# Performance work log

Hardware: AMD Instinct MI355X
Metric: run time of the kernel (lower is better)

## Reference

```python
import jax, jax.numpy as jnp
import numpy as np

N = 50000
E = 800000
D_IN, D_HID, D_OUT = 128, 128, 64


def setup_inputs() -> dict:
    key = jax.random.key(0)
    ks = jax.random.split(key, 8)
    x = jax.random.normal(ks[0], (N, D_IN), dtype=jnp.float32)
    edge_index = jax.random.randint(ks[1], (2, E), 0, N, dtype=jnp.int64)
    # Glorot-ish init for weights
    W1 = jax.random.normal(ks[2], (D_IN, D_HID), dtype=jnp.float32) / np.sqrt(D_IN)
    b1 = jnp.zeros((D_HID,), dtype=jnp.float32)
    W2 = jax.random.normal(ks[3], (D_HID, D_OUT), dtype=jnp.float32) / np.sqrt(D_HID)
    b2 = jnp.zeros((D_OUT,), dtype=jnp.float32)
    fc_W = jax.random.normal(ks[4], (D_OUT, D_OUT), dtype=jnp.float32) / np.sqrt(D_OUT)
    fc_b = jnp.zeros((D_OUT,), dtype=jnp.float32)
    return {"x": x, "edge_index": edge_index, "W1": W1, "b1": b1,
            "W2": W2, "b2": b2, "fc_W": fc_W, "fc_b": fc_b}


def _gcn_norm(edge_index, n_nodes):
    # PyG GCNConv default: add self-loops, symmetric normalization
    src, dst = edge_index[0], edge_index[1]
    loops = jnp.arange(n_nodes, dtype=edge_index.dtype)
    src = jnp.concatenate([src, loops])
    dst = jnp.concatenate([dst, loops])
    deg = jax.ops.segment_sum(jnp.ones_like(dst, dtype=jnp.float32), dst,
                              num_segments=n_nodes)
    dinv = jnp.where(deg > 0, jax.lax.rsqrt(deg), 0.0)
    norm = dinv[src] * dinv[dst]  # [E + N]
    return src, dst, norm


def _gcn_conv(x, src, dst, norm, W, b):
    h = x @ W                          # [N, d_out] transform first (fewer FLOPs)
    msg = h[src] * norm[:, None]       # gather + scale  [E+N, d_out]
    out = jax.ops.segment_sum(msg, dst, num_segments=x.shape[0])
    return out + b


def reference(x, edge_index, W1, b1, W2, b2, fc_W, fc_b):
    src, dst, norm = _gcn_norm(edge_index, x.shape[0])
    h = jax.nn.relu(_gcn_conv(x, src, dst, norm, W1, b1))
    h = jax.nn.relu(_gcn_conv(h, src, dst, norm, W2, b2))
    return h @ fc_W + fc_b
```

## Files before the change

### kernel.cpp

```cpp
#include <hip/hip_runtime.h>
#include <hip/hip_bf16.h>


typedef __attribute__((ext_vector_type(8))) short bf16x8;
typedef __attribute__((ext_vector_type(4))) float f32x4;

#define SLAB 64
#define BCAP 6144
#define BINCH 4096
#define BINR (BINCH / 1024)

__device__ __forceinline__ unsigned short f2bf(float f) {
    unsigned u = __float_as_uint(f);
    unsigned r = (u + 0x7FFFu + ((u >> 16) & 1u)) >> 16;
    return (unsigned short)r;
}
__device__ __forceinline__ float bf16_lo(unsigned u) {
    return __uint_as_float((u & 0xFFFFu) << 16);
}
__device__ __forceinline__ float bf16_hi(unsigned u) {
    return __uint_as_float(u & 0xFFFF0000u);
}

#define UNPK16(cA, cB, ci)                                        \
    ci[0] = cA.x & 0xFFFFu;  ci[1] = cA.x >> 16;                  \
    ci[2] = cA.y & 0xFFFFu;  ci[3] = cA.y >> 16;                  \
    ci[4] = cA.z & 0xFFFFu;  ci[5] = cA.z >> 16;                  \
    ci[6] = cA.w & 0xFFFFu;  ci[7] = cA.w >> 16;                  \
    ci[8] = cB.x & 0xFFFFu;  ci[9] = cB.x >> 16;                  \
    ci[10] = cB.y & 0xFFFFu; ci[11] = cB.y >> 16;                 \
    ci[12] = cB.z & 0xFFFFu; ci[13] = cB.z >> 16;                 \
    ci[14] = cB.w & 0xFFFFu; ci[15] = cB.w >> 16;


__global__ void k_wt(const float* __restrict__ W1, const float* __restrict__ W2,
                     const float* __restrict__ fcW,
                     unsigned short* __restrict__ W1T, unsigned short* __restrict__ W2T,
                     unsigned short* __restrict__ fcWT, int* __restrict__ gcnt,
                     unsigned short* __restrict__ hs1r, unsigned short* __restrict__ hs2,
                     int n) {
    int j = blockIdx.x * blockDim.x + threadIdx.x;
    if (j < 256) gcnt[j] = 0;
    if (j < 16384) {
        int m = j >> 7, k = j & 127;
        W1T[j] = f2bf(W1[k * 128 + m]);
    } else if (j < 24576) {
        int q = j - 16384;
        int m = q >> 7, k = q & 127;
        W2T[q] = f2bf(W2[k * 64 + m]);
    } else if (j < 28672) {
        int q = j - 24576;
        int m = q >> 6, k = q & 63;
        fcWT[q] = f2bf(fcW[k * 64 + m]);
    } else if (j < 28800) {
        hs1r[(size_t)n * 128 + (j - 28672)] = 0;
    } else if (j < 28864) {
        hs2[(size_t)n * 64 + (j - 28800)] = 0;
    }
}


__device__ __forceinline__ void gemm1_body(const float* __restrict__ X,
                                           const unsigned short* __restrict__ W1T,
                                           unsigned short* __restrict__ outp,
                                           int n, int blk, int tid,
                                           unsigned short* xs) {
    constexpr int LDW = 136;
    int base = blk * 64;
    for (int idx = tid; idx < 64 * 32; idx += 256) {
        int r = idx >> 5, c = idx & 31;
        int row = base + r;
        float4 v = make_float4(0.f, 0.f, 0.f, 0.f);
        if (row < n) v = ((const float4*)X)[(size_t)row * 32 + c];
        unsigned short* dp = &xs[r * LDW + c * 4];
        dp[0] = f2bf(v.x); dp[1] = f2bf(v.y); dp[2] = f2bf(v.z); dp[3] = f2bf(v.w);
    }
    __syncthreads();

    int wave = tid >> 6, lane = tid & 63;
    int quad = lane >> 4, l16 = lane & 15;
    int rbase = wave * 16;

    bf16x8 af[4];
#pragma unroll
    for (int kb = 0; kb < 4; ++kb)
        af[kb] = *(const bf16x8*)&xs[(rbase + l16) * LDW + kb * 32 + quad * 8];

    f32x4 accs[8];
#pragma unroll
    for (int jt = 0; jt < 8; ++jt) {
        f32x4 acc = {0.f, 0.f, 0.f, 0.f};
#pragma unroll
        for (int kb = 0; kb < 4; ++kb) {
            bf16x8 bf = *(const bf16x8*)&W1T[(size_t)(jt * 16 + l16) * 128 + kb * 32 + quad * 8];
            acc = __builtin_amdgcn_mfma_f32_16x16x32_bf16(af[kb], bf, acc, 0, 0, 0);
        }
        accs[jt] = acc;
    }
    __syncthreads();

#pragma unroll
    for (int jt = 0; jt < 8; ++jt)
#pragma unroll
        for (int r = 0; r < 4; ++r)
            xs[(rbase + quad * 4 + r) * LDW + jt * 16 + l16] = f2bf(accs[jt][r]);
    __syncthreads();
    for (int idx = tid; idx < 64 * 16; idx += 256) {
        int r = idx >> 4, cc = idx & 15;
        int row = base + r;
        if (row < n) {
            uint4 v = *(const uint4*)&xs[r * LDW + cc * 8];
            *(uint4*)&outp[(size_t)row * 128 + cc * 8] = v;
        }
    }
}


__global__ __launch_bounds__(1024) void k_front(
    const int* __restrict__ src, const int* __restrict__ dst, int e,
    int* __restrict__ gcnt, unsigned* __restrict__ staging,
    const float* __restrict__ x, const unsigned short* __restrict__ W1T,
    unsigned short* __restrict__ hs1r, int n, int nbk, int ngemm) {
    __shared__ __align__(16) unsigned short xs4[4][64 * 136];
    __shared__ int bcnt[256], bpos[256], gofs[256];
    int bid = (int)blockIdx.x, tid = (int)threadIdx.x;

    if (bid < ngemm) {
        int tile = tid >> 8;
        gemm1_body(x, W1T, hs1r, n, bid * 4 + tile, tid & 255, xs4[tile]);
    } else {
        int b0 = bid - ngemm;
        if (tid < 256) { bcnt[tid] = 0; bpos[tid] = 0; }
        __syncthreads();
        int e0 = b0 * BINCH;
        int d[BINR], s[BINR];
#pragma unroll
        for (int r = 0; r < BINR; ++r) {
            int i = e0 + r * 1024 + tid;
            if (i < e) { d[r] = dst[i]; s[r] = src[i]; } else d[r] = -1;
        }
#pragma unroll
        for (int r = 0; r < BINR; ++r)
            if (d[r] >= 0) atomicAdd(&bcnt[d[r] >> 8], 1);
        __syncthreads();
        if (tid < nbk) {
            int c = bcnt[tid];
            gofs[tid] = c ? atomicAdd(&gcnt[tid], c) : 0;
        }
        __syncthreads();
#pragma unroll
        for (int r = 0; r < BINR; ++r) {
            if (d[r] >= 0) {
                int b = d[r] >> 8;
                int p = atomicAdd(&bpos[b], 1);
                int idx = gofs[b] + p;
                if (idx < BCAP)
                    staging[(size_t)b * BCAP + idx] =
                        ((unsigned)d[r] << 16) | (unsigned)s[r];
            }
        }
    }
}


__global__ __launch_bounds__(1024) void k_scatter(
    const unsigned* __restrict__ staging, const int* __restrict__ gcnt,
    int* __restrict__ cnt, unsigned short* __restrict__ col,
    float* __restrict__ dinv, unsigned* __restrict__ hs1u, int n) {
    __shared__ int lcnt[256];
    __shared__ __align__(16) unsigned short ls[256 * SLAB];
    __shared__ float sdi[256];
    int b = (int)blockIdx.x, t = (int)threadIdx.x;
    if (t < 256) lcnt[t] = 0;
    unsigned sent2 = (unsigned)n | ((unsigned)n << 16);
    for (int i = t; i < 256 * SLAB / 2; i += 1024) ((unsigned*)ls)[i] = sent2;
    __syncthreads();
    int eb = gcnt[b]; if (eb > BCAP) eb = BCAP;
    const unsigned* sp = staging + (size_t)b * BCAP;
    for (int i = t; i < eb; i += 1024) {
        unsigned pk = sp[i];
        int dl = (int)(pk >> 16) & 255;
        int pos = atomicAdd(&lcnt[dl], 1);
        if (pos < SLAB) ls[(dl << 6) + pos] = (unsigned short)(pk & 0xFFFFu);
    }
    __syncthreads();
    int base = b << 8;
    const uint4* lsv = (const uint4*)ls;
    uint4* gv = (uint4*)(col + ((size_t)base << 6));
    for (int i = t; i < 256 * SLAB / 8; i += 1024) gv[i] = lsv[i];
    if (t < 256) {
        int c = lcnt[t];
        float dv = rsqrtf((float)c + 1.0f);
        sdi[t] = dv;
        cnt[base + t] = c;
        dinv[base + t] = dv;
    }
    __syncthreads();
    int rows = n - base; if (rows > 256) rows = 256; if (rows < 0) rows = 0;
    unsigned* hp = hs1u + ((size_t)base << 6);
    for (int i = t; i < rows * 64; i += 1024) {
        int r = i >> 6;
        unsigned u = hp[i];
        float sc = sdi[r];
        unsigned lo = f2bf(sc * bf16_lo(u));
        unsigned hi = f2bf(sc * bf16_hi(u));
        hp[i] = lo | (hi << 16);
    }
}


__global__ __launch_bounds__(256) void k_aggg128(
    const int* __restrict__ cnt, const unsigned short* __restrict__ col,
    const unsigned short* __restrict__ hs, const float* __restrict__ dinv,
    const float* __restrict__ bias, const unsigned short* __restrict__ W2T,
    unsigned short* __restrict__ hs2, int n) {
    __shared__ __align__(16) unsigned short ys[16 * 136];
    __shared__ float ldi[16];
    int tid = (int)threadIdx.x;
    int w = tid >> 6, lane = tid & 63;
    int q = lane >> 4, l16 = lane & 15;
    int gbase = (int)blockIdx.x * 16;
    const uint4* hp4 = (const uint4*)hs;

    int node = gbase + w * 4 + q;
    int c = cnt[node]; if (c > SLAB) c = SLAB;

    const unsigned short* cp = &col[(size_t)node * SLAB];
    float di = dinv[node];
    int h0 = node < n ? node : n;
    uint4 su = hp4[(size_t)h0 * 16 + l16];
    float a0 = bf16_lo(su.x), a1 = bf16_hi(su.x);
    float a2 = bf16_lo(su.y), a3 = bf16_hi(su.y);
    float a4 = bf16_lo(su.z), a5 = bf16_hi(su.z);
    float a6 = bf16_lo(su.w), a7 = bf16_hi(su.w);

    uint4 cA = *(const uint4*)&cp[0];
    uint4 cB = *(const uint4*)&cp[8];
    for (int i = 0; i < c; i += 16) {
        int nx = (i + 16) & 63;
        uint4 nA = *(const uint4*)&cp[nx];
        uint4 nB = *(const uint4*)&cp[nx + 8];
        unsigned ci[16];
        UNPK16(cA, cB, ci)
        uint4 u[16];
#pragma unroll
        for (int j = 0; j < 16; ++j) u[j] = hp4[(size_t)ci[j] * 16 + l16];
#pragma unroll
        for (int j = 0; j < 16; ++j) {
            a0 += bf16_lo(u[j].x); a1 += bf16_hi(u[j].x);
            a2 += bf16_lo(u[j].y); a3 += bf16_hi(u[j].y);
            a4 += bf16_lo(u[j].z); a5 += bf16_hi(u[j].z);
            a6 += bf16_lo(u[j].w); a7 += bf16_hi(u[j].w);
        }
        cA = nA; cB = nB;
    }

    float4 bv0 = *(const float4*)&bias[l16 * 8];
    float4 bv1 = *(const float4*)&bias[l16 * 8 + 4];
    float v0 = fmaxf(di * a0 + bv0.x, 0.0f);
    float v1 = fmaxf(di * a1 + bv0.y, 0.0f);
    float v2 = fmaxf(di * a2 + bv0.z, 0.0f);
    float v3 = fmaxf(di * a3 + bv0.w, 0.0f);
    float v4 = fmaxf(di * a4 + bv1.x, 0.0f);
    float v5 = fmaxf(di * a5 + bv1.y, 0.0f);
    float v6 = fmaxf(di * a6 + bv1.z, 0.0f);
    float v7 = fmaxf(di * a7 + bv1.w, 0.0f);
    uint4 ov;
    ov.x = (unsigned)f2bf(v0) | ((unsigned)f2bf(v1) << 16);
    ov.y = (unsigned)f2bf(v2) | ((unsigned)f2bf(v3) << 16);
    ov.z = (unsigned)f2bf(v4) | ((unsigned)f2bf(v5) << 16);
    ov.w = (unsigned)f2bf(v6) | ((unsigned)f2bf(v7) << 16);
    *(uint4*)((char*)ys + (size_t)(w * 4 + q) * 272 + l16 * 16) = ov;
    if (l16 == 0) ldi[w * 4 + q] = di;
    __syncthreads();

    int quad = lane >> 4, l16b = lane & 15;
    bf16x8 a[4];
#pragma unroll
    for (int kb = 0; kb < 4; ++kb)
        a[kb] = *(const bf16x8*)&ys[l16b * 136 + kb * 32 + quad * 8];
    f32x4 acc = {0.f, 0.f, 0.f, 0.f};
#pragma unroll
    for (int kb = 0; kb < 4; ++kb) {
        bf16x8 bf = *(const bf16x8*)&W2T[(size_t)(w * 16 + l16b) * 128 + kb * 32 + quad * 8];
        acc = __builtin_amdgcn_mfma_f32_16x16x32_bf16(a[kb], bf, acc, 0, 0, 0);
    }
#pragma unroll
    for (int r = 0; r < 4; ++r) {
        int lrow = quad * 4 + r;
        int row = gbase + lrow;
        if (row < n)
            hs2[(size_t)row * 64 + w * 16 + l16b] = f2bf(acc[r] * ldi[lrow]);
    }
}


__global__ __launch_bounds__(256) void k_aggg64(
    const int* __restrict__ cnt, const unsigned short* __restrict__ col,
    const unsigned short* __restrict__ hs, const float* __restrict__ dinv,
    const float* __restrict__ bias, const unsigned short* __restrict__ fcWT,
    const float* __restrict__ fcb, float* __restrict__ out, int n) {
    __shared__ __align__(16) unsigned short yt[16 * 72];
    int tid = (int)threadIdx.x;
    int w = tid >> 6, lane = tid & 63;
    int q = lane >> 4, l16 = lane & 15;
    int gbase = (int)blockIdx.x * 16;
    const uint2* hp2 = (const uint2*)hs;

    int node = gbase + w * 4 + q;
    int c = cnt[node]; if (c > SLAB) c = SLAB;

    const unsigned short* cp = &col[(size_t)node * SLAB];
    float di = dinv[node];
    int h0 = node < n ? node : n;
    uint2 su = hp2[(size_t)h0 * 16 + l16];
    float a0 = bf16_lo(su.x), a1 = bf16_hi(su.x);
    float a2 = bf16_lo(su.y), a3 = bf16_hi(su.y);

    uint4 cA = *(const uint4*)&cp[0];
    uint4 cB = *(const uint4*)&cp[8];
    for (int i = 0; i < c; i += 16) {
        int nx = (i + 16) & 63;
        uint4 nA = *(const uint4*)&cp[nx];
        uint4 nB = *(const uint4*)&cp[nx + 8];
        unsigned ci[16];
        UNPK16(cA, cB, ci)
        uint2 u[16];
#pragma unroll
        for (int j = 0; j < 16; ++j) u[j] = hp2[(size_t)ci[j] * 16 + l16];
#pragma unroll
        for (int j = 0; j < 16; ++j) {
            a0 += bf16_lo(u[j].x); a1 += bf16_hi(u[j].x);
            a2 += bf16_lo(u[j].y); a3 += bf16_hi(u[j].y);
        }
        cA = nA; cB = nB;
    }

    float4 bv = *(const float4*)&bias[l16 * 4];
    float v0 = fmaxf(di * a0 + bv.x, 0.0f);
    float v1 = fmaxf(di * a1 + bv.y, 0.0f);
    float v2 = fmaxf(di * a2 + bv.z, 0.0f);
    float v3 = fmaxf(di * a3 + bv.w, 0.0f);
    uint2 ov;
    ov.x = (unsigned)f2bf(v0) | ((unsigned)f2bf(v1) << 16);
    ov.y = (unsigned)f2bf(v2) | ((unsigned)f2bf(v3) << 16);
    *(uint2*)((char*)yt + (size_t)(w * 4 + q) * 144 + l16 * 8) = ov;
    __syncthreads();

    int quad = lane >> 4, l16b = lane & 15;
    bf16x8 a[2];
#pragma unroll
    for (int kb = 0; kb < 2; ++kb)
        a[kb] = *(const bf16x8*)&yt[l16b * 72 + kb * 32 + quad * 8];
    f32x4 acc = {0.f, 0.f, 0.f, 0.f};
#pragma unroll
    for (int kb = 0; kb < 2; ++kb) {
        bf16x8 bf = *(const bf16x8*)&fcWT[(size_t)(w * 16 + l16b) * 64 + kb * 32 + quad * 8];
        acc = __builtin_amdgcn_mfma_f32_16x16x32_bf16(a[kb], bf, acc, 0, 0, 0);
    }
    float bv2 = fcb[w * 16 + l16b];
#pragma unroll
    for (int r = 0; r < 4; ++r) {
        int row = gbase + quad * 4 + r;
        if (row < n)
            out[(size_t)row * 64 + w * 16 + l16b] = acc[r] + bv2;
    }
}


extern "C" void kernel_launch(void* const* d_in, const int* in_sizes, int n_in,
                              void* d_out, int out_size, void* d_ws, size_t ws_size,
                              hipStream_t stream) {
    const float* x   = (const float*)d_in[0];
    const int*   ei  = (const int*)d_in[1];
    const float* W1  = (const float*)d_in[2];
    const float* b1  = (const float*)d_in[3];
    const float* W2  = (const float*)d_in[4];
    const float* b2  = (const float*)d_in[5];
    const float* fcW = (const float*)d_in[6];
    const float* fcb = (const float*)d_in[7];
    float* out = (float*)d_out;

    const int N = in_sizes[0] / 128;
    const int E = in_sizes[1] / 2;
    const int* src = ei;
    const int* dst = ei + E;

    const int NB    = (N + 255) >> 8;
    const int Npad  = NB << 8;
    const int nbin  = (E + BINCH - 1) / BINCH;
    const int gg64  = (N + 63) / 64;
    const int ngemm = (gg64 + 3) / 4;
    const int nagg  = (N + 15) / 16;

    auto align16 = [](size_t v) { return (v + 15) & ~(size_t)15; };
    char* p = (char*)d_ws;
    int* gcnt = (int*)p;                       p += align16(sizeof(int) * 256);
    unsigned* staging = (unsigned*)p;          p += align16(sizeof(unsigned) * (size_t)NB * BCAP);
    int* cnt = (int*)p;                        p += align16(sizeof(int) * Npad);
    float* dinv = (float*)p;                   p += align16(sizeof(float) * Npad);
    unsigned short* col = (unsigned short*)p;  p += align16(sizeof(unsigned short) * (size_t)Npad * SLAB);
    unsigned short* W1T = (unsigned short*)p;  p += align16(2 * 128 * 128);
    unsigned short* W2T = (unsigned short*)p;  p += align16(2 * 64 * 128);
    unsigned short* fcWT = (unsigned short*)p; p += align16(2 * 64 * 64);
    unsigned short* hs1r = (unsigned short*)p; p += align16(2 * ((size_t)N + 1) * 128);
    unsigned short* hs2 = (unsigned short*)p;  p += align16(2 * ((size_t)N + 1) * 64);

    k_wt<<<114, 256, 0, stream>>>(W1, W2, fcW, W1T, W2T, fcWT, gcnt,
                                  hs1r, hs2, N);

    k_front<<<ngemm + nbin, 1024, 0, stream>>>(src, dst, E, gcnt, staging,
                                               x, W1T, hs1r, N, NB, ngemm);
    k_scatter<<<NB, 1024, 0, stream>>>(staging, gcnt, cnt, col, dinv,
                                       (unsigned*)hs1r, N);

    k_aggg128<<<nagg, 256, 0, stream>>>(cnt, col, hs1r, dinv, b1, W2T, hs2, N);

    k_aggg64<<<nagg, 256, 0, stream>>>(cnt, col, hs2, dinv, b2, fcWT, fcb, out, N);
}
```

Measured before the change: 172.2 us.

## Regroup preprocessing: fuse edge binning with weight prep, GEMM with CSR scatter

```diff
diff --git a/kernel.cpp b/kernel.cpp
--- a/kernel.cpp
+++ b/kernel.cpp
@@ -33,29 +33,66 @@
     ci[14] = cB.w & 0xFFFFu; ci[15] = cB.w >> 16;
 
 
-__global__ void k_wt(const float* __restrict__ W1, const float* __restrict__ W2,
-                     const float* __restrict__ fcW,
-                     unsigned short* __restrict__ W1T, unsigned short* __restrict__ W2T,
-                     unsigned short* __restrict__ fcWT, int* __restrict__ gcnt,
-                     unsigned short* __restrict__ hs1r, unsigned short* __restrict__ hs2,
-                     int n) {
-    int j = blockIdx.x * blockDim.x + threadIdx.x;
-    if (j < 256) gcnt[j] = 0;
-    if (j < 16384) {
-        int m = j >> 7, k = j & 127;
-        W1T[j] = f2bf(W1[k * 128 + m]);
-    } else if (j < 24576) {
-        int q = j - 16384;
-        int m = q >> 7, k = q & 127;
-        W2T[q] = f2bf(W2[k * 64 + m]);
-    } else if (j < 28672) {
-        int q = j - 24576;
-        int m = q >> 6, k = q & 63;
-        fcWT[q] = f2bf(fcW[k * 64 + m]);
-    } else if (j < 28800) {
-        hs1r[(size_t)n * 128 + (j - 28672)] = 0;
-    } else if (j < 28864) {
-        hs2[(size_t)n * 64 + (j - 28800)] = 0;
+__global__ __launch_bounds__(1024) void k_init(
+    const int* __restrict__ src, const int* __restrict__ dst, int e,
+    int* __restrict__ gcnt, unsigned* __restrict__ staging,
+    const float* __restrict__ W1, const float* __restrict__ W2,
+    const float* __restrict__ fcW,
+    unsigned short* __restrict__ W1T, unsigned short* __restrict__ W2T,
+    unsigned short* __restrict__ fcWT,
+    unsigned short* __restrict__ hs1r, unsigned short* __restrict__ hs2,
+    int n, int nbk, int nbin) {
+    __shared__ int bcnt[256], bpos[256], gofs[256];
+    int bid = (int)blockIdx.x, tid = (int)threadIdx.x;
+
+    if (bid < nbin) {
+        if (tid < 256) { bcnt[tid] = 0; bpos[tid] = 0; }
+        __syncthreads();
+        int e0 = bid * BINCH;
+        int d[BINR], s[BINR];
+#pragma unroll
+        for (int r = 0; r < BINR; ++r) {
+            int i = e0 + r * 1024 + tid;
+            if (i < e) { d[r] = dst[i]; s[r] = src[i]; } else d[r] = -1;
+        }
+#pragma unroll
+        for (int r = 0; r < BINR; ++r)
+            if (d[r] >= 0) atomicAdd(&bcnt[d[r] >> 8], 1);
+        __syncthreads();
+        if (tid < nbk) {
+            int c = bcnt[tid];
+            gofs[tid] = c ? atomicAdd(&gcnt[tid], c) : 0;
+        }
+        __syncthreads();
+#pragma unroll
+        for (int r = 0; r < BINR; ++r) {
+            if (d[r] >= 0) {
+                int b = d[r] >> 8;
+                int p = atomicAdd(&bpos[b], 1);
+                int idx = gofs[b] + p;
+                if (idx < BCAP)
+                    staging[(size_t)b * BCAP + idx] =
+                        ((unsigned)d[r] << 16) | (unsigned)s[r];
+            }
+        }
+    } else {
+        int j = (bid - nbin) * 1024 + tid;
+        if (j < 16384) {
+            int m = j >> 7, k = j & 127;
+            W1T[j] = f2bf(W1[k * 128 + m]);
+        } else if (j < 24576) {
+            int q = j - 16384;
+            int m = q >> 7, k = q & 127;
+            W2T[q] = f2bf(W2[k * 64 + m]);
+        } else if (j < 28672) {
+            int q = j - 24576;
+            int m = q >> 6, k = q & 63;
+            fcWT[q] = f2bf(fcW[k * 64 + m]);
+        } else if (j < 28800) {
+            hs1r[(size_t)n * 128 + (j - 28672)] = 0;
+        } else if (j < 28864) {
+            hs2[(size_t)n * 64 + (j - 28800)] = 0;
+        }
     }
 }
 
@@ -116,95 +153,45 @@
 }
 
 
-__global__ __launch_bounds__(1024) void k_front(
-    const int* __restrict__ src, const int* __restrict__ dst, int e,
-    int* __restrict__ gcnt, unsigned* __restrict__ staging,
+__global__ __launch_bounds__(1024) void k_gemsc(
     const float* __restrict__ x, const unsigned short* __restrict__ W1T,
-    unsigned short* __restrict__ hs1r, int n, int nbk, int ngemm) {
-    __shared__ __align__(16) unsigned short xs4[4][64 * 136];
-    __shared__ int bcnt[256], bpos[256], gofs[256];
+    unsigned short* __restrict__ hs1r,
+    const unsigned* __restrict__ staging, const int* __restrict__ gcnt,
+    int* __restrict__ cnt, unsigned short* __restrict__ col,
+    float* __restrict__ dinv, int n, int ngemm) {
+    __shared__ __align__(16) unsigned char smem[69632];
     int bid = (int)blockIdx.x, tid = (int)threadIdx.x;
 
     if (bid < ngemm) {
         int tile = tid >> 8;
-        gemm1_body(x, W1T, hs1r, n, bid * 4 + tile, tid & 255, xs4[tile]);
+        unsigned short* xs = (unsigned short*)(smem + tile * 17408);
+        gemm1_body(x, W1T, hs1r, n, bid * 4 + tile, tid & 255, xs);
     } else {
-        int b0 = bid - ngemm;
-        if (tid < 256) { bcnt[tid] = 0; bpos[tid] = 0; }
+        int* lcnt = (int*)smem;
+        unsigned short* ls = (unsigned short*)(smem + 1024);
+        int b = bid - ngemm, t = tid;
+        if (t < 256) lcnt[t] = 0;
+        unsigned sent2 = (unsigned)n | ((unsigned)n << 16);
+        for (int i = t; i < 256 * SLAB / 2; i += 1024) ((unsigned*)ls)[i] = sent2;
         __syncthreads();
-        int e0 = b0 * BINCH;
-        int d[BINR], s[BINR];
-#pragma unroll
-        for (int r = 0; r < BINR; ++r) {
-            int i = e0 + r * 1024 + tid;
-            if (i < e) { d[r] = dst[i]; s[r] = src[i]; } else d[r] = -1;
-        }
-#pragma unroll
-        for (int r = 0; r < BINR; ++r)
-            if (d[r] >= 0) atomicAdd(&bcnt[d[r] >> 8], 1);
+        int eb = gcnt[b]; if (eb > BCAP) eb = BCAP;
+        const unsigned* sp = staging + (size_t)b * BCAP;
+        for (int i = t; i < eb; i += 1024) {
+            unsigned pk = sp[i];
+            int dl = (int)(pk >> 16) & 255;
+            int pos = atomicAdd(&lcnt[dl], 1);
+            if (pos < SLAB) ls[(dl << 6) + pos] = (unsigned short)(pk & 0xFFFFu);
+        }
         __syncthreads();
-        if (tid < nbk) {
-            int c = bcnt[tid];
-            gofs[tid] = c ? atomicAdd(&gcnt[tid], c) : 0;
-        }
-        __syncthreads();
-#pragma unroll
-        for (int r = 0; r < BINR; ++r) {
-            if (d[r] >= 0) {
-                int b = d[r] >> 8;
-                int p = atomicAdd(&bpos[b], 1);
-                int idx = gofs[b] + p;
-                if (idx < BCAP)
-                    staging[(size_t)b * BCAP + idx] =
-                        ((unsigned)d[r] << 16) | (unsigned)s[r];
-            }
-        }
-    }
-}
-
-
-__global__ __launch_bounds__(1024) void k_scatter(
-    const unsigned* __restrict__ staging, const int* __restrict__ gcnt,
-    int* __restrict__ cnt, unsigned short* __restrict__ col,
-    float* __restrict__ dinv, unsigned* __restrict__ hs1u, int n) {
-    __shared__ int lcnt[256];
-    __shared__ __align__(16) unsigned short ls[256 * SLAB];
-    __shared__ float sdi[256];
-    int b = (int)blockIdx.x, t = (int)threadIdx.x;
-    if (t < 256) lcnt[t] = 0;
-    unsigned sent2 = (unsigned)n | ((unsigned)n << 16);
-    for (int i = t; i < 256 * SLAB / 2; i += 1024) ((unsigned*)ls)[i] = sent2;
-    __syncthreads();
-    int eb = gcnt[b]; if (eb > BCAP) eb = BCAP;
-    const unsigned* sp = staging + (size_t)b * BCAP;
-    for (int i = t; i < eb; i += 1024) {
-        unsigned pk = sp[i];
-        int dl = (int)(pk >> 16) & 255;
-        int pos = atomicAdd(&lcnt[dl], 1);
-        if (pos < SLAB) ls[(dl << 6) + pos] = (unsigned short)(pk & 0xFFFFu);
-    }
-    __syncthreads();
-    int base = b << 8;
-    const uint4* lsv = (const uint4*)ls;
-    uint4* gv = (uint4*)(col + ((size_t)base << 6));
-    for (int i = t; i < 256 * SLAB / 8; i += 1024) gv[i] = lsv[i];
-    if (t < 256) {
-        int c = lcnt[t];
-        float dv = rsqrtf((float)c + 1.0f);
-        sdi[t] = dv;
-        cnt[base + t] = c;
-        dinv[base + t] = dv;
-    }
-    __syncthreads();
-    int rows = n - base; if (rows > 256) rows = 256; if (rows < 0) rows = 0;
-    unsigned* hp = hs1u + ((size_t)base << 6);
-    for (int i = t; i < rows * 64; i += 1024) {
-        int r = i >> 6;
-        unsigned u = hp[i];
-        float sc = sdi[r];
-        unsigned lo = f2bf(sc * bf16_lo(u));
-        unsigned hi = f2bf(sc * bf16_hi(u));
-        hp[i] = lo | (hi << 16);
+        int base = b << 8;
+        const uint4* lsv = (const uint4*)ls;
+        uint4* gv = (uint4*)(col + ((size_t)base << 6));
+        for (int i = t; i < 256 * SLAB / 8; i += 1024) gv[i] = lsv[i];
+        if (t < 256) {
+            int c = lcnt[t];
+            cnt[base + t] = c;
+            dinv[base + t] = rsqrtf((float)c + 1.0f);
+        }
     }
 }
 
@@ -227,12 +214,11 @@
 
     const unsigned short* cp = &col[(size_t)node * SLAB];
     float di = dinv[node];
-    int h0 = node < n ? node : n;
-    uint4 su = hp4[(size_t)h0 * 16 + l16];
-    float a0 = bf16_lo(su.x), a1 = bf16_hi(su.x);
-    float a2 = bf16_lo(su.y), a3 = bf16_hi(su.y);
-    float a4 = bf16_lo(su.z), a5 = bf16_hi(su.z);
-    float a6 = bf16_lo(su.w), a7 = bf16_hi(su.w);
+    uint4 su = hp4[(size_t)node * 16 + l16];
+    float a0 = di * bf16_lo(su.x), a1 = di * bf16_hi(su.x);
+    float a2 = di * bf16_lo(su.y), a3 = di * bf16_hi(su.y);
+    float a4 = di * bf16_lo(su.z), a5 = di * bf16_hi(su.z);
+    float a6 = di * bf16_lo(su.w), a7 = di * bf16_hi(su.w);
 
     uint4 cA = *(const uint4*)&cp[0];
     uint4 cB = *(const uint4*)&cp[8];
@@ -245,12 +231,15 @@
         uint4 u[16];
 #pragma unroll
         for (int j = 0; j < 16; ++j) u[j] = hp4[(size_t)ci[j] * 16 + l16];
+        float dw[16];
+#pragma unroll
+        for (int j = 0; j < 16; ++j) dw[j] = dinv[ci[j]];
 #pragma unroll
         for (int j = 0; j < 16; ++j) {
-            a0 += bf16_lo(u[j].x); a1 += bf16_hi(u[j].x);
-            a2 += bf16_lo(u[j].y); a3 += bf16_hi(u[j].y);
-            a4 += bf16_lo(u[j].z); a5 += bf16_hi(u[j].z);
-            a6 += bf16_lo(u[j].w); a7 += bf16_hi(u[j].w);
+            a0 = fmaf(dw[j], bf16_lo(u[j].x), a0); a1 = fmaf(dw[j], bf16_hi(u[j].x), a1);
+            a2 = fmaf(dw[j], bf16_lo(u[j].y), a2); a3 = fmaf(dw[j], bf16_hi(u[j].y), a3);
+            a4 = fmaf(dw[j], bf16_lo(u[j].z), a4); a5 = fmaf(dw[j], bf16_hi(u[j].z), a5);
+            a6 = fmaf(dw[j], bf16_lo(u[j].w), a6); a7 = fmaf(dw[j], bf16_hi(u[j].w), a7);
         }
         cA = nA; cB = nB;
     }
@@ -312,8 +301,7 @@
 
     const unsigned short* cp = &col[(size_t)node * SLAB];
     float di = dinv[node];
-    int h0 = node < n ? node : n;
-    uint2 su = hp2[(size_t)h0 * 16 + l16];
+    uint2 su = hp2[(size_t)node * 16 + l16];
     float a0 = bf16_lo(su.x), a1 = bf16_hi(su.x);
     float a2 = bf16_lo(su.y), a3 = bf16_hi(su.y);
 
@@ -389,6 +377,7 @@
     const int NB    = (N + 255) >> 8;
     const int Npad  = NB << 8;
     const int nbin  = (E + BINCH - 1) / BINCH;
+    const int nwt   = (28864 + 1023) / 1024;
     const int gg64  = (N + 63) / 64;
     const int ngemm = (gg64 + 3) / 4;
     const int nagg  = (N + 15) / 16;
@@ -406,13 +395,14 @@
     unsigned short* hs1r = (unsigned short*)p; p += align16(2 * ((size_t)N + 1) * 128);
     unsigned short* hs2 = (unsigned short*)p;  p += align16(2 * ((size_t)N + 1) * 64);
 
-    k_wt<<<114, 256, 0, stream>>>(W1, W2, fcW, W1T, W2T, fcWT, gcnt,
-                                  hs1r, hs2, N);
-
-    k_front<<<ngemm + nbin, 1024, 0, stream>>>(src, dst, E, gcnt, staging,
-                                               x, W1T, hs1r, N, NB, ngemm);
-    k_scatter<<<NB, 1024, 0, stream>>>(staging, gcnt, cnt, col, dinv,
-                                       (unsigned*)hs1r, N);
+    hipMemsetAsync(gcnt, 0, sizeof(int) * 256, stream);
+
+    k_init<<<nbin + nwt, 1024, 0, stream>>>(src, dst, E, gcnt, staging,
+                                            W1, W2, fcW, W1T, W2T, fcWT,
+                                            hs1r, hs2, N, NB, nbin);
+
+    k_gemsc<<<ngemm + NB, 1024, 0, stream>>>(x, W1T, hs1r, staging, gcnt,
+                                             cnt, col, dinv, N, ngemm);
 
     k_aggg128<<<nagg, 256, 0, stream>>>(cnt, col, hs1r, dinv, b1, W2T, hs2, N);
 
```

Measured after the change: 177.9 us. +3.3%, slower.
